# Kernel tuning notes

Hardware: AMD Instinct MI355X
Metric: run time of the kernel (lower is better)

## Reference

```python
import jax, jax.numpy as jnp
import numpy as np

N, D_IN, D_OUT = 8192, 1024, 1024

def setup_inputs() -> dict:
    key = jax.random.key(0)
    k0, k1, k2, k3 = jax.random.split(key, 4)
    scale = 1.0 / np.sqrt(D_IN)
    return {
        "inputs": jax.random.normal(k0, (N, D_IN), dtype=jnp.float32),
        "W_q": jax.random.uniform(k1, (D_IN, D_OUT), jnp.float32, -scale, scale),
        "W_k": jax.random.uniform(k2, (D_IN, D_OUT), jnp.float32, -scale, scale),
        "W_v": jax.random.uniform(k3, (D_IN, D_OUT), jnp.float32, -scale, scale),
    }

def reference(inputs, W_q, W_k, W_v):
    # Linear projections (no bias): [N, d_out]
    q = inputs @ W_q
    k = inputs @ W_k
    v = inputs @ W_v
    d_k = k.shape[-1]
    # Full N x N scores, scaled softmax over last axis
    scores = (q @ k.T) / jnp.sqrt(jnp.asarray(d_k, q.dtype))
    attn = jax.nn.softmax(scores, axis=-1)
    return attn @ v
```

## Files before the change

kernel.cpp:

```cpp
#include <hip/hip_runtime.h>
#include <hip/hip_fp16.h>
#include <stdint.h>


typedef _Float16 half_t;
typedef _Float16 half8 __attribute__((ext_vector_type(8)));
typedef _Float16 half4 __attribute__((ext_vector_type(4)));
typedef float f32x4 __attribute__((ext_vector_type(4)));
typedef int i32x4 __attribute__((ext_vector_type(4)));

#define GLOAD16(gp, lp)                                                        \
  __builtin_amdgcn_global_load_lds(                                            \
      (__attribute__((address_space(1))) void*)(gp),                           \
      (__attribute__((address_space(3))) void*)(lp), 16, 0, 0)

#define BAR() __builtin_amdgcn_s_barrier()
#define VMCNT8() asm volatile("s_waitcnt vmcnt(8)")
#define VMCNT4() asm volatile("s_waitcnt vmcnt(4)")
#define VMCNT0() asm volatile("s_waitcnt vmcnt(0)")

__global__ __launch_bounds__(256) void cast_f32_to_f16(
    const float* __restrict__ in, half_t* __restrict__ out, int n4) {
  int i = blockIdx.x * 256 + threadIdx.x;
  if (i < n4) {
    float4 v = ((const float4*)in)[i];
    half4 o = {(half_t)v.x, (half_t)v.y, (half_t)v.z, (half_t)v.w};
    ((half4*)out)[i] = o;
  }
}

template <typename Tin>
__global__ __launch_bounds__(256) void transpose_cast(
    const Tin* __restrict__ in, int ldin, half_t* __restrict__ out, int ldout,
    int R, int C) {
  __shared__ half_t tile[64][65];
  const int c0 = blockIdx.x * 64, r0 = blockIdx.y * 64;
  const int tx = threadIdx.x & 63, ty = threadIdx.x >> 6;
#pragma unroll
  for (int i = 0; i < 16; i++) {
    int r = ty * 16 + i;
    tile[r][tx] = (half_t)in[(size_t)(r0 + r) * ldin + c0 + tx];
  }
  __syncthreads();
#pragma unroll
  for (int i = 0; i < 16; i++) {
    int c = ty * 16 + i;
    out[(size_t)(c0 + c) * ldout + r0 + tx] = tile[tx][c];
  }
}

__global__ __launch_bounds__(256) void rowsum_recip(
    const float* __restrict__ rowpart, float* __restrict__ rinv, int rows,
    int w4) {
  int r = blockIdx.x * 256 + threadIdx.x;
  if (r < rows) {
    const float4* p = (const float4*)(rowpart + (size_t)r * (w4 * 4));
    float s = 0.f;
    for (int i = 0; i < w4; i++) {
      float4 v = p[i];
      s += v.x + v.y + v.z + v.w;
    }
    rinv[r] = 1.f / s;
  }
}

__global__ __launch_bounds__(256) void reduce_add2h(
    const half8* __restrict__ a, const half8* __restrict__ b,
    float4* __restrict__ o, int n8) {
  int i = blockIdx.x * 256 + threadIdx.x;
  if (i < n8) {
    half8 x = a[i], y = b[i];
    float4 o0, o1;
    o0.x = (float)x[0] + (float)y[0];
    o0.y = (float)x[1] + (float)y[1];
    o0.z = (float)x[2] + (float)y[2];
    o0.w = (float)x[3] + (float)y[3];
    o1.x = (float)x[4] + (float)y[4];
    o1.y = (float)x[5] + (float)y[5];
    o1.z = (float)x[6] + (float)y[6];
    o1.w = (float)x[7] + (float)y[7];
    o[2 * i] = o0;
    o[2 * i + 1] = o1;
  }
}

template <typename To, int MODE>
__global__ __launch_bounds__(512, 2) void gemm256(
    const half_t* __restrict__ A, int lda, const half_t* __restrict__ Bt,
    int ldb, To* __restrict__ C, int ldc, int M, int N, int K, int ychunks,
    int SG, const float* __restrict__ rinv, int8_t* __restrict__ qi8,
    int8_t* __restrict__ ki8) {
  __shared__ __align__(16) char sm[131072];

  const int t = threadIdx.x;
  const int w = t >> 6;
  const int ln = t & 63;

  const int nwg = gridDim.x * gridDim.y;
  const int bid = blockIdx.y * gridDim.x + blockIdx.x;
  const int cpx = nwg >> 3;
  const int q = (bid & 7) * cpx + (bid >> 3);
  const int tiles_y = gridDim.y / ychunks;
  const int per_chunk = gridDim.x * tiles_y;
  const int chunk = q / per_chunk;
  int r_ = q - chunk * per_chunk;
  const int sw = SG * tiles_y;
  const int s_ = r_ / sw;
  r_ -= s_ * sw;
  const int by = r_ / SG;
  const int bx = s_ * SG + (r_ - by * SG);

  A += (size_t)chunk * K;
  Bt += (size_t)chunk * K;
  C += (size_t)chunk * M * ldc;

  const int row0 = by * 256;
  const int col0 = bx * 256;

  const int srow = w * 8 + (ln >> 3);
  const int sslot = (ln & 7) ^ ((ln >> 3) & 7);
  const half_t* Ag = A + (size_t)(row0 + srow) * lda + sslot * 8;
  const half_t* Bg = Bt + (size_t)(col0 + srow) * ldb + sslot * 8;
  const int ldsw = w * 1024;

#define STAGE_AB(kt, bb)                                                       \
  do {                                                                         \
    const half_t* ga_ = Ag + (size_t)(kt) * 64;                                \
    const half_t* gb_ = Bg + (size_t)(kt) * 64;                                \
    GLOAD16(ga_, sm + (bb) + ldsw);                                            \
    GLOAD16(ga_ + 64 * (size_t)lda, sm + (bb) + 8192 + ldsw);                  \
    GLOAD16(ga_ + 128 * (size_t)lda, sm + (bb) + 16384 + ldsw);                \
    GLOAD16(ga_ + 192 * (size_t)lda, sm + (bb) + 24576 + ldsw);                \
    GLOAD16(gb_, sm + (bb) + 32768 + ldsw);                                    \
    GLOAD16(gb_ + 64 * (size_t)ldb, sm + (bb) + 40960 + ldsw);                 \
    GLOAD16(gb_ + 128 * (size_t)ldb, sm + (bb) + 49152 + ldsw);                \
    GLOAD16(gb_ + 192 * (size_t)ldb, sm + (bb) + 57344 + ldsw);                \
  } while (0)

  const int wr = w >> 2;
  const int wc = w & 3;
  const int fr = ln & 15;
  const int kg = ln >> 4;
  const int sx0 = ((kg ^ (fr & 7)) << 4);
  const int sx1 = sx0 ^ 64;
  const int arow = (wr * 128 + fr) * 128;
  const int brow = 32768 + (wc * 64 + fr) * 128;

#define READ_A(MI0, cb)                                                        \
  _Pragma("unroll") for (int mi = 0; mi < 4; mi++) {                           \
    a4[mi][0] = *(const half8*)(sm + (cb) + arow + (MI0 + mi) * 2048 + sx0);   \
    a4[mi][1] = *(const half8*)(sm + (cb) + arow + (MI0 + mi) * 2048 + sx1);   \
  }
#define READ_B(NI, cb)                                                         \
  do {                                                                         \
    b8[NI][0] = *(const half8*)(sm + (cb) + brow + (NI) * 2048 + sx0);         \
    b8[NI][1] = *(const half8*)(sm + (cb) + brow + (NI) * 2048 + sx1);         \
  } while (0)

#define MFMA_Q(MI0, NI0)                                                       \
  __builtin_amdgcn_s_setprio(1);                                               \
  _Pragma("unroll") for (int kk = 0; kk < 2; kk++)                             \
  _Pragma("unroll") for (int mi = 0; mi < 4; mi++)                             \
  _Pragma("unroll") for (int ni = 0; ni < 2; ni++)                             \
      acc[MI0 + mi][NI0 + ni] = __builtin_amdgcn_mfma_f32_16x16x32_f16(        \
          a4[mi][kk], b8[NI0 + ni][kk], acc[MI0 + mi][NI0 + ni], 0, 0, 0);     \
  __builtin_amdgcn_s_setprio(0);

  half8 a4[4][2], b8[4][2];
  f32x4 acc[8][4] = {};

  const int NT = K >> 6;

  STAGE_AB(0, 0);
  STAGE_AB(1, 65536);
  VMCNT8();
  BAR();

#define TILE(tt, cb)                                                           \
  do {                                                                         \
    READ_A(0, cb);                                                             \
    READ_B(0, cb);                                                             \
    READ_B(1, cb);                                                             \
    BAR();                                                                     \
    MFMA_Q(0, 0);                                                              \
    BAR();                                                                     \
    READ_B(2, cb);                                                             \
    READ_B(3, cb);                                                             \
    BAR();                                                                     \
    MFMA_Q(0, 2);                                                              \
    BAR();                                                                     \
    READ_A(4, cb);                                                             \
    BAR();                                                                     \
    MFMA_Q(4, 2);                                                              \
    BAR();                                                                     \
    if ((tt) + 2 < NT) {                                                       \
      STAGE_AB((tt) + 2, cb);                                                  \
      VMCNT8();                                                                \
    } else {                                                                   \
      VMCNT0();                                                                \
    }                                                                          \
    BAR();                                                                     \
    MFMA_Q(4, 0);                                                              \
    BAR();                                                                     \
  } while (0)

  for (int kt = 0; kt < NT; kt += 2) {
    TILE(kt, 0);
    TILE(kt + 1, 65536);
  }

  const int orow = row0 + wr * 128 + (ln >> 4) * 4;
  const int ocol = col0 + wc * 64 + (ln & 15);
  if constexpr (MODE == 2) {
    if (bx < 8) {
      int8_t* qk = bx < 4 ? qi8 : ki8;
      const int cbase = ocol - (bx < 4 ? 0 : 1024);
#pragma unroll
      for (int mi = 0; mi < 8; mi++)
#pragma unroll
        for (int j = 0; j < 4; j++) {
          const size_t r = orow + mi * 16 + j;
#pragma unroll
          for (int ni = 0; ni < 4; ni++) {
            float f = acc[mi][ni][j] * 32.f;
            f = fminf(fmaxf(f, -127.f), 127.f);
            qk[r * 1024 + cbase + ni * 16] = (int8_t)rintf(f);
          }
        }
    } else {
      const int cbase = ocol - 2048;
#pragma unroll
      for (int mi = 0; mi < 8; mi++)
#pragma unroll
        for (int ni = 0; ni < 4; ni++) {
          To* cp = C + (size_t)(orow + mi * 16) * ldc + cbase + ni * 16;
#pragma unroll
          for (int j = 0; j < 4; j++) cp[(size_t)j * ldc] = (To)acc[mi][ni][j];
        }
    }
  } else if constexpr (MODE == 3) {
#pragma unroll
    for (int mi = 0; mi < 8; mi++)
#pragma unroll
      for (int j = 0; j < 4; j++) {
        const size_t r = orow + mi * 16 + j;
        const float s = rinv[r];
#pragma unroll
        for (int ni = 0; ni < 4; ni++)
          C[r * ldc + ocol + ni * 16] = (To)(acc[mi][ni][j] * s);
      }
  } else {
#pragma unroll
    for (int mi = 0; mi < 8; mi++)
#pragma unroll
      for (int ni = 0; ni < 4; ni++) {
        To* cp = C + (size_t)(orow + mi * 16) * ldc + ocol + ni * 16;
#pragma unroll
        for (int j = 0; j < 4; j++) cp[(size_t)j * ldc] = (To)acc[mi][ni][j];
      }
  }
#undef TILE
#undef MFMA_Q
#undef READ_A
#undef READ_B
#undef STAGE_AB
}

__global__ __launch_bounds__(512, 2) void gemm256_i8exp(
    const int8_t* __restrict__ A, int lda, const int8_t* __restrict__ Bt,
    int ldb, half_t* __restrict__ C, int ldc, int K, int SG,
    float* __restrict__ rowpart) {
  __shared__ __align__(16) char sm[65536];

  const int t = threadIdx.x;
  const int w = t >> 6;
  const int ln = t & 63;

  const int nwg = gridDim.x * gridDim.y;
  const int bid = blockIdx.y * gridDim.x + blockIdx.x;
  const int cpx = nwg >> 3;
  const int q = (bid & 7) * cpx + (bid >> 3);
  const int sw = SG * gridDim.y;
  const int s_ = q / sw;
  int r_ = q - s_ * sw;
  const int by = r_ / SG;
  const int bx = s_ * SG + (r_ - by * SG);

  const int row0 = by * 256;
  const int col0 = bx * 256;

  const int rt = w * 16 + (ln >> 2);
  const int sl = (ln & 3) ^ ((rt >> 1) & 3);
  const int8_t* Ag = A + (size_t)(row0 + rt) * lda + sl * 16;
  const int8_t* Bg = Bt + (size_t)(col0 + rt) * ldb + sl * 16;
  const int ldsw = w * 1024;

#define STAGE8(kt, bb)                                                         \
  do {                                                                         \
    const int8_t* ga_ = Ag + (size_t)(kt) * 64;                                \
    const int8_t* gb_ = Bg + (size_t)(kt) * 64;                                \
    GLOAD16(ga_, sm + (bb) + ldsw);                                            \
    GLOAD16(ga_ + 128 * (size_t)lda, sm + (bb) + 8192 + ldsw);                 \
    GLOAD16(gb_, sm + (bb) + 16384 + ldsw);                                    \
    GLOAD16(gb_ + 128 * (size_t)ldb, sm + (bb) + 24576 + ldsw);                \
  } while (0)

  const int wr = w >> 2;
  const int wc = w & 3;
  const int fr = ln & 15;
  const int kg = ln >> 4;
  const int sx = (kg ^ ((fr >> 1) & 3)) << 4;
  const int arow = (wr * 128 + fr) * 64;
  const int brow = 16384 + (wc * 64 + fr) * 64;

#define READ_A8(MI0, cb)                                                       \
  _Pragma("unroll") for (int mi = 0; mi < 4; mi++)                             \
      a8[mi] = *(const i32x4*)(sm + (cb) + arow + (MI0 + mi) * 1024 + sx);
#define READ_B8(NI, cb)                                                        \
  b8v[NI] = *(const i32x4*)(sm + (cb) + brow + (NI) * 1024 + sx);

#define MFMA_Q8(MI0, NI0)                                                      \
  __builtin_amdgcn_s_setprio(1);                                               \
  _Pragma("unroll") for (int mi = 0; mi < 4; mi++)                             \
  _Pragma("unroll") for (int ni = 0; ni < 2; ni++)                             \
      acc[MI0 + mi][NI0 + ni] = __builtin_amdgcn_mfma_i32_16x16x64_i8(         \
          a8[mi], b8v[NI0 + ni], acc[MI0 + mi][NI0 + ni], 0, 0, 0);            \
  __builtin_amdgcn_s_setprio(0);

  i32x4 a8[4], b8v[4];
  i32x4 acc[8][4] = {};

  const int NT = K >> 6;

  STAGE8(0, 0);
  STAGE8(1, 32768);
  VMCNT4();
  BAR();

#define TILE8(tt, cb)                                                          \
  do {                                                                         \
                                                                       \
    READ_A8(0, cb);                                                            \
    READ_B8(0, cb);                                                            \
    READ_B8(1, cb);                                                            \
    READ_B8(2, cb);                                                            \
    READ_B8(3, cb);                                                            \
    MFMA_Q8(0, 0);                                                             \
    MFMA_Q8(0, 2);                                                             \
                                                                       \
    READ_A8(4, cb);                                                            \
    MFMA_Q8(4, 2);                                                             \
    BAR();        \
    if ((tt) + 2 < NT) {                                                       \
      STAGE8((tt) + 2, cb);                                                    \
      MFMA_Q8(4, 0);                                                           \
      VMCNT4();                     \
    } else {                                                                   \
      MFMA_Q8(4, 0);                                                           \
      VMCNT0();                                                                \
    }                                                                          \
    BAR();                             \
  } while (0)

  for (int kt = 0; kt < NT; kt += 2) {
    TILE8(kt, 0);
    TILE8(kt + 1, 32768);
  }

  const int orow = row0 + wr * 128 + (ln >> 4) * 4;
  const int ocol = col0 + wc * 64 + (ln & 15);
  const float sc = 3.0517578125e-5f;
  const int rp_ld = gridDim.x * 4;
#pragma unroll
  for (int mi = 0; mi < 8; mi++) {
#pragma unroll
    for (int j = 0; j < 4; j++) {
      const int r = orow + mi * 16 + j;
      float s = 0.f;
#pragma unroll
      for (int ni = 0; ni < 4; ni++) {
        float e = __expf((float)acc[mi][ni][j] * sc);
        C[(size_t)r * ldc + ocol + ni * 16] = (half_t)e;
        s += e;
      }
      s += __shfl_xor(s, 1);
      s += __shfl_xor(s, 2);
      s += __shfl_xor(s, 4);
      s += __shfl_xor(s, 8);
      if ((ln & 15) == 0) rowpart[(size_t)r * rp_ld + bx * 4 + wc] = s;
    }
  }
#undef TILE8
#undef MFMA_Q8
#undef READ_A8
#undef READ_B8
#undef STAGE8
}

extern "C" void kernel_launch(void* const* d_in, const int* in_sizes, int n_in,
                              void* d_out, int out_size, void* d_ws,
                              size_t ws_size, hipStream_t stream) {
  const float* X = (const float*)d_in[0];
  const float* Wq = (const float*)d_in[1];
  const float* Wk = (const float*)d_in[2];
  const float* Wv = (const float*)d_in[3];
  float* out = (float*)d_out;

  const int N = 8192, D = 1024;

  char* ws = (char*)d_ws;
  half_t* Xh   = (half_t*)(ws);
  half_t* Wth  = (half_t*)(ws + (16ull << 20));
  half_t* Vh   = (half_t*)(ws + (22ull << 20));
  half_t* partH= (half_t*)(ws + (38ull << 20));
  int8_t* Qi8  = (int8_t*)(ws + (70ull << 20));
  int8_t* Ki8  = (int8_t*)(ws + (78ull << 20));
  half_t* Vt   = (half_t*)(ws + (70ull << 20));
  half_t* S    = (half_t*)(ws + (86ull << 20));
  float* rowpart = (float*)ws;
  float* rinv    = (float*)(ws + (4ull << 20));

  cast_f32_to_f16<<<(N * D / 4 + 255) / 256, 256, 0, stream>>>(X, Xh, N * D / 4);

  dim3 tg(D / 64, D / 64);
  transpose_cast<float><<<tg, 256, 0, stream>>>(Wq, D, Wth + 0ull * D * D, D, D, D);
  transpose_cast<float><<<tg, 256, 0, stream>>>(Wk, D, Wth + 1ull * D * D, D, D, D);
  transpose_cast<float><<<tg, 256, 0, stream>>>(Wv, D, Wth + 2ull * D * D, D, D, D);

  gemm256<half_t, 2><<<dim3(3 * D / 256, N / 256), 512, 0, stream>>>(
      Xh, D, Wth, D, Vh, D, N, 3 * D, D, 1, 4, nullptr, Qi8, Ki8);

  gemm256_i8exp<<<dim3(N / 256, N / 256), 512, 0, stream>>>(
      Qi8, D, Ki8, D, S, N, D, 8, rowpart);

  rowsum_recip<<<(N + 255) / 256, 256, 0, stream>>>(rowpart, rinv, N, 32);

  transpose_cast<half_t><<<dim3(D / 64, N / 64), 256, 0, stream>>>(
      Vh, D, Vt, N, N, D);

  gemm256<half_t, 3><<<dim3(D / 256, 2 * N / 256), 512, 0, stream>>>(
      S, N, Vt, N, partH, D, N, D, N / 2, 2, 4, rinv, nullptr, nullptr);

  reduce_add2h<<<(N * D / 8 + 255) / 256, 256, 0, stream>>>(
      (const half8*)partH, (const half8*)(partH + (size_t)N * D), (float4*)out,
      N * D / 8);
}
```

Before: 322.6 us.

## Software-pipeline LDS fragment reads against MFMA in both GEMM mainloops

Restructures the f16 and int8 GEMM inner loops to double-buffer register fragments, so the LDS reads for the next quarter or tile are issued before the current MFMA block runs. It also prefetches the next tile's first A/B fragments right after the staging barrier. Most intra-tile barriers are dropped and replaced with sched_barrier and explicit lgkmcnt waits. This should hide LDS latency behind matrix math and cut barrier stalls, at the cost of more live VGPRs and a risk of lower occupancy or spills.

```diff
diff --git a/kernel.cpp b/kernel.cpp
--- a/kernel.cpp
+++ b/kernel.cpp
@@ -15,6 +15,8 @@
       (__attribute__((address_space(3))) void*)(lp), 16, 0, 0)
 
 #define BAR() __builtin_amdgcn_s_barrier()
+#define SCHED0() __builtin_amdgcn_sched_barrier(0)
+#define LGKM0() asm volatile("s_waitcnt lgkmcnt(0)")
 #define VMCNT8() asm volatile("s_waitcnt vmcnt(8)")
 #define VMCNT4() asm volatile("s_waitcnt vmcnt(4)")
 #define VMCNT0() asm volatile("s_waitcnt vmcnt(0)")
@@ -146,27 +148,22 @@
   const int arow = (wr * 128 + fr) * 128;
   const int brow = 32768 + (wc * 64 + fr) * 128;
 
-#define READ_A(MI0, cb)                                                        \
-  _Pragma("unroll") for (int mi = 0; mi < 4; mi++) {                           \
-    a4[mi][0] = *(const half8*)(sm + (cb) + arow + (MI0 + mi) * 2048 + sx0);   \
-    a4[mi][1] = *(const half8*)(sm + (cb) + arow + (MI0 + mi) * 2048 + sx1);   \
-  }
-#define READ_B(NI, cb)                                                         \
-  do {                                                                         \
-    b8[NI][0] = *(const half8*)(sm + (cb) + brow + (NI) * 2048 + sx0);         \
-    b8[NI][1] = *(const half8*)(sm + (cb) + brow + (NI) * 2048 + sx1);         \
-  } while (0)
-
-#define MFMA_Q(MI0, NI0)                                                       \
+#define RD_A(dst, MI0, cb, SX)                                                 \
+  _Pragma("unroll") for (int mi = 0; mi < 4; mi++) dst[mi] =                   \
+      *(const half8*)(sm + (cb) + arow + ((MI0) + mi) * 2048 + (SX));
+#define RD_B(dst, cb, SX)                                                      \
+  _Pragma("unroll") for (int ni = 0; ni < 4; ni++) dst[ni] =                   \
+      *(const half8*)(sm + (cb) + brow + ni * 2048 + (SX));
+
+#define MM16(MI0, As, Bs)                                                      \
   __builtin_amdgcn_s_setprio(1);                                               \
-  _Pragma("unroll") for (int kk = 0; kk < 2; kk++)                             \
   _Pragma("unroll") for (int mi = 0; mi < 4; mi++)                             \
-  _Pragma("unroll") for (int ni = 0; ni < 2; ni++)                             \
-      acc[MI0 + mi][NI0 + ni] = __builtin_amdgcn_mfma_f32_16x16x32_f16(        \
-          a4[mi][kk], b8[NI0 + ni][kk], acc[MI0 + mi][NI0 + ni], 0, 0, 0);     \
+  _Pragma("unroll") for (int ni = 0; ni < 4; ni++)                             \
+      acc[(MI0) + mi][ni] = __builtin_amdgcn_mfma_f32_16x16x32_f16(            \
+          As[mi], Bs[ni], acc[(MI0) + mi][ni], 0, 0, 0);                       \
   __builtin_amdgcn_s_setprio(0);
 
-  half8 a4[4][2], b8[4][2];
+  half8 Aa[4], Ab[4], Bb0[4], Bb1[4];
   f32x4 acc[8][4] = {};
 
   const int NT = K >> 6;
@@ -175,23 +172,26 @@
   STAGE_AB(1, 65536);
   VMCNT8();
   BAR();
+  RD_A(Aa, 0, 0, sx0);
+  RD_B(Bb0, 0, sx0);
 
 #define TILE(tt, cb)                                                           \
   do {                                                                         \
-    READ_A(0, cb);                                                             \
-    READ_B(0, cb);                                                             \
-    READ_B(1, cb);                                                             \
-    BAR();                                                                     \
-    MFMA_Q(0, 0);                                                              \
-    BAR();                                                                     \
-    READ_B(2, cb);                                                             \
-    READ_B(3, cb);                                                             \
-    BAR();                                                                     \
-    MFMA_Q(0, 2);                                                              \
-    BAR();                                                                     \
-    READ_A(4, cb);                                                             \
-    BAR();                                                                     \
-    MFMA_Q(4, 2);                                                              \
+                                                              \
+    RD_A(Ab, 4, cb, sx0);                                                      \
+    SCHED0();                                                                  \
+    MM16(0, Aa, Bb0);                                                          \
+                                                              \
+    RD_A(Aa, 0, cb, sx1);                                                      \
+    RD_B(Bb1, cb, sx1);                                                        \
+    SCHED0();                                                                  \
+    MM16(4, Ab, Bb0);                                                          \
+                                                              \
+    RD_A(Ab, 4, cb, sx1);                                                      \
+    SCHED0();                                                                  \
+    MM16(0, Aa, Bb1);                                                          \
+                \
+    LGKM0();                                                                   \
     BAR();                                                                     \
     if ((tt) + 2 < NT) {                                                       \
       STAGE_AB((tt) + 2, cb);                                                  \
@@ -200,8 +200,13 @@
       VMCNT0();                                                                \
     }                                                                          \
     BAR();                                                                     \
-    MFMA_Q(4, 0);                                                              \
-    BAR();                                                                     \
+                \
+    if ((tt) + 1 < NT) {                                                       \
+      RD_A(Aa, 0, (cb) ^ 65536, sx0);                                          \
+      RD_B(Bb0, (cb) ^ 65536, sx0);                                            \
+    }                                                                          \
+    SCHED0();                                                                  \
+    MM16(4, Ab, Bb1);                                                          \
   } while (0)
 
   for (int kt = 0; kt < NT; kt += 2) {
@@ -260,9 +265,9 @@
       }
   }
 #undef TILE
-#undef MFMA_Q
-#undef READ_A
-#undef READ_B
+#undef MM16
+#undef RD_A
+#undef RD_B
 #undef STAGE_AB
 }
 
@@ -313,21 +318,22 @@
   const int arow = (wr * 128 + fr) * 64;
   const int brow = 16384 + (wc * 64 + fr) * 64;
 
-#define READ_A8(MI0, cb)                                                       \
-  _Pragma("unroll") for (int mi = 0; mi < 4; mi++)                             \
-      a8[mi] = *(const i32x4*)(sm + (cb) + arow + (MI0 + mi) * 1024 + sx);
-#define READ_B8(NI, cb)                                                        \
-  b8v[NI] = *(const i32x4*)(sm + (cb) + brow + (NI) * 1024 + sx);
-
-#define MFMA_Q8(MI0, NI0)                                                      \
+#define RD_A8(dst, MI0, cb)                                                    \
+  _Pragma("unroll") for (int mi = 0; mi < 4; mi++) dst[mi] =                   \
+      *(const i32x4*)(sm + (cb) + arow + ((MI0) + mi) * 1024 + sx);
+#define RD_B8(dst, cb)                                                         \
+  _Pragma("unroll") for (int ni = 0; ni < 4; ni++) dst[ni] =                   \
+      *(const i32x4*)(sm + (cb) + brow + ni * 1024 + sx);
+
+#define MM16_8(MI0, As, Bs)                                                    \
   __builtin_amdgcn_s_setprio(1);                                               \
   _Pragma("unroll") for (int mi = 0; mi < 4; mi++)                             \
-  _Pragma("unroll") for (int ni = 0; ni < 2; ni++)                             \
-      acc[MI0 + mi][NI0 + ni] = __builtin_amdgcn_mfma_i32_16x16x64_i8(         \
-          a8[mi], b8v[NI0 + ni], acc[MI0 + mi][NI0 + ni], 0, 0, 0);            \
+  _Pragma("unroll") for (int ni = 0; ni < 4; ni++)                             \
+      acc[(MI0) + mi][ni] = __builtin_amdgcn_mfma_i32_16x16x64_i8(             \
+          As[mi], Bs[ni], acc[(MI0) + mi][ni], 0, 0, 0);                       \
   __builtin_amdgcn_s_setprio(0);
 
-  i32x4 a8[4], b8v[4];
+  i32x4 Aa8[4], Ab8[4], B0s[4], B1s[4];
   i32x4 acc[8][4] = {};
 
   const int NT = K >> 6;
@@ -336,35 +342,37 @@
   STAGE8(1, 32768);
   VMCNT4();
   BAR();
-
-#define TILE8(tt, cb)                                                          \
+  RD_A8(Aa8, 0, 0);
+  RD_B8(B0s, 0);
+
+#define TILE8(tt, cb, Bc, Bn)                                                  \
   do {                                                                         \
-                                                                       \
-    READ_A8(0, cb);                                                            \
-    READ_B8(0, cb);                                                            \
-    READ_B8(1, cb);                                                            \
-    READ_B8(2, cb);                                                            \
-    READ_B8(3, cb);                                                            \
-    MFMA_Q8(0, 0);                                                             \
-    MFMA_Q8(0, 2);                                                             \
-                                                                       \
-    READ_A8(4, cb);                                                            \
-    MFMA_Q8(4, 2);                                                             \
-    BAR();        \
+                                                                 \
+    RD_A8(Ab8, 4, cb);                                                         \
+    SCHED0();                                                                  \
+    MM16_8(0, Aa8, Bc);                                                        \
+                                                                 \
+    LGKM0();                                                                   \
+    BAR();                                                                     \
     if ((tt) + 2 < NT) {                                                       \
       STAGE8((tt) + 2, cb);                                                    \
-      MFMA_Q8(4, 0);                                                           \
-      VMCNT4();                     \
+      VMCNT4();                                                                \
     } else {                                                                   \
-      MFMA_Q8(4, 0);                                                           \
       VMCNT0();                                                                \
     }                                                                          \
-    BAR();                             \
+    BAR();                                                                     \
+                       \
+    if ((tt) + 1 < NT) {                                                       \
+      RD_A8(Aa8, 0, (cb) ^ 32768);                                             \
+      RD_B8(Bn, (cb) ^ 32768);                                                 \
+    }                                                                          \
+    SCHED0();                                                                  \
+    MM16_8(4, Ab8, Bc);                                                        \
   } while (0)
 
   for (int kt = 0; kt < NT; kt += 2) {
-    TILE8(kt, 0);
-    TILE8(kt + 1, 32768);
+    TILE8(kt, 0, B0s, B1s);
+    TILE8(kt + 1, 32768, B1s, B0s);
   }
 
   const int orow = row0 + wr * 128 + (ln >> 4) * 4;
@@ -391,9 +399,9 @@
     }
   }
 #undef TILE8
-#undef MFMA_Q8
-#undef READ_A8
-#undef READ_B8
+#undef MM16_8
+#undef RD_A8
+#undef RD_B8
 #undef STAGE8
 }
 
```

After: 573.5 us. 77.8% more time.

## Write V transposed from projection epilogue and use dedicated K=32 f16 PV GEMM

Applied to the files above, without the earlier changes.

The projection GEMM epilogue now writes V directly in transposed layout as 4-element half vectors, which removes the separate V transpose kernel and its extra pass over memory. The P·V product moves to a new gemm256_h32 kernel that uses the 16x16x32 f16 MFMA with a double-buffered 32-wide K tile and applies the row reciprocal in the epilogue. The transposed V stores are strided by N, so they may coalesce poorly. The new kernel's pipelining also differs from the generic gemm256 path.

```diff
diff --git a/kernel.cpp b/kernel.cpp
--- a/kernel.cpp
+++ b/kernel.cpp
@@ -228,27 +228,16 @@
           }
         }
     } else {
-      const int cbase = ocol - 2048;
 #pragma unroll
       for (int mi = 0; mi < 8; mi++)
 #pragma unroll
         for (int ni = 0; ni < 4; ni++) {
-          To* cp = C + (size_t)(orow + mi * 16) * ldc + cbase + ni * 16;
-#pragma unroll
-          for (int j = 0; j < 4; j++) cp[(size_t)j * ldc] = (To)acc[mi][ni][j];
+          const int c = ocol - 2048 + ni * 16;
+          half4 v = {(half_t)acc[mi][ni][0], (half_t)acc[mi][ni][1],
+                     (half_t)acc[mi][ni][2], (half_t)acc[mi][ni][3]};
+          *(half4*)(C + (size_t)c * ldc + orow + mi * 16) = v;
         }
     }
-  } else if constexpr (MODE == 3) {
-#pragma unroll
-    for (int mi = 0; mi < 8; mi++)
-#pragma unroll
-      for (int j = 0; j < 4; j++) {
-        const size_t r = orow + mi * 16 + j;
-        const float s = rinv[r];
-#pragma unroll
-        for (int ni = 0; ni < 4; ni++)
-          C[r * ldc + ocol + ni * 16] = (To)(acc[mi][ni][j] * s);
-      }
   } else {
 #pragma unroll
     for (int mi = 0; mi < 8; mi++)
@@ -264,6 +253,134 @@
 #undef READ_A
 #undef READ_B
 #undef STAGE_AB
+}
+
+__global__ __launch_bounds__(512, 2) void gemm256_h32(
+    const half_t* __restrict__ A, int lda, const half_t* __restrict__ Bt,
+    int ldb, half_t* __restrict__ C, int ldc, int M, int K, int ychunks,
+    int SG, const float* __restrict__ rinv) {
+  __shared__ __align__(16) char sm[65536];
+
+  const int t = threadIdx.x;
+  const int w = t >> 6;
+  const int ln = t & 63;
+
+  const int nwg = gridDim.x * gridDim.y;
+  const int bid = blockIdx.y * gridDim.x + blockIdx.x;
+  const int cpx = nwg >> 3;
+  const int q = (bid & 7) * cpx + (bid >> 3);
+  const int tiles_y = gridDim.y / ychunks;
+  const int per_chunk = gridDim.x * tiles_y;
+  const int chunk = q / per_chunk;
+  int r_ = q - chunk * per_chunk;
+  const int sw = SG * tiles_y;
+  const int s_ = r_ / sw;
+  r_ -= s_ * sw;
+  const int by = r_ / SG;
+  const int bx = s_ * SG + (r_ - by * SG);
+
+  A += (size_t)chunk * K;
+  Bt += (size_t)chunk * K;
+  C += (size_t)chunk * M * ldc;
+
+  const int row0 = by * 256;
+  const int col0 = bx * 256;
+
+  const int rt = w * 16 + (ln >> 2);
+  const int sl = (ln & 3) ^ ((rt >> 1) & 3);
+  const half_t* Ag = A + (size_t)(row0 + rt) * lda + sl * 8;
+  const half_t* Bg = Bt + (size_t)(col0 + rt) * ldb + sl * 8;
+  const int ldsw = w * 1024;
+
+#define STAGEH(kt, bb)                                                         \
+  do {                                                                         \
+    const half_t* ga_ = Ag + (size_t)(kt) * 32;                                \
+    const half_t* gb_ = Bg + (size_t)(kt) * 32;                                \
+    GLOAD16(ga_, sm + (bb) + ldsw);                                            \
+    GLOAD16(ga_ + 128 * (size_t)lda, sm + (bb) + 8192 + ldsw);                 \
+    GLOAD16(gb_, sm + (bb) + 16384 + ldsw);                                    \
+    GLOAD16(gb_ + 128 * (size_t)ldb, sm + (bb) + 24576 + ldsw);                \
+  } while (0)
+
+  const int wr = w >> 2;
+  const int wc = w & 3;
+  const int fr = ln & 15;
+  const int kg = ln >> 4;
+  const int sx = (kg ^ ((fr >> 1) & 3)) << 4;
+  const int arow = (wr * 128 + fr) * 64;
+  const int brow = 16384 + (wc * 64 + fr) * 64;
+
+#define RDH_A(MI0, cb)                                                         \
+  _Pragma("unroll") for (int mi = 0; mi < 4; mi++)                             \
+      ah[mi] = *(const half8*)(sm + (cb) + arow + ((MI0) + mi) * 1024 + sx);
+#define RDH_B(NI, cb)                                                          \
+  bh[NI] = *(const half8*)(sm + (cb) + brow + (NI) * 1024 + sx);
+
+#define MMH_Q(MI0, NI0)                                                        \
+  __builtin_amdgcn_s_setprio(1);                                               \
+  _Pragma("unroll") for (int mi = 0; mi < 4; mi++)                             \
+  _Pragma("unroll") for (int ni = 0; ni < 2; ni++)                             \
+      acc[(MI0) + mi][(NI0) + ni] = __builtin_amdgcn_mfma_f32_16x16x32_f16(    \
+          ah[mi], bh[(NI0) + ni], acc[(MI0) + mi][(NI0) + ni], 0, 0, 0);       \
+  __builtin_amdgcn_s_setprio(0);
+
+  half8 ah[4], bh[4];
+  f32x4 acc[8][4] = {};
+
+  const int NT = K >> 5;
+
+  STAGEH(0, 0);
+  STAGEH(1, 32768);
+  VMCNT4();
+  BAR();
+
+#define TILEH(tt, cb)                                                          \
+  do {                                                                         \
+                                                                       \
+    RDH_A(0, cb);                                                              \
+    RDH_B(0, cb);                                                              \
+    RDH_B(1, cb);                                                              \
+    RDH_B(2, cb);                                                              \
+    RDH_B(3, cb);                                                              \
+    MMH_Q(0, 0);                                                               \
+    MMH_Q(0, 2);                                                               \
+                                                                       \
+    RDH_A(4, cb);                                                              \
+    MMH_Q(4, 2);                                                               \
+    BAR();                    \
+    if ((tt) + 2 < NT) {                                                       \
+      STAGEH((tt) + 2, cb);                                                    \
+      MMH_Q(4, 0);                                                             \
+      VMCNT4();                     \
+    } else {                                                                   \
+      MMH_Q(4, 0);                                                             \
+      VMCNT0();                                                                \
+    }                                                                          \
+    BAR();                                          \
+  } while (0)
+
+  for (int kt = 0; kt < NT; kt += 2) {
+    TILEH(kt, 0);
+    TILEH(kt + 1, 32768);
+  }
+
+  const int orow = row0 + wr * 128 + (ln >> 4) * 4;
+  const int ocol = col0 + wc * 64 + (ln & 15);
+#pragma unroll
+  for (int mi = 0; mi < 8; mi++)
+#pragma unroll
+    for (int j = 0; j < 4; j++) {
+      const size_t r = orow + mi * 16 + j;
+      const float s = rinv[r];
+#pragma unroll
+      for (int ni = 0; ni < 4; ni++)
+        C[r * ldc + ocol + ni * 16] = (half_t)(acc[mi][ni][j] * s);
+    }
+#undef TILEH
+#undef MMH_Q
+#undef RDH_A
+#undef RDH_B
+#undef STAGEH
 }
 
 __global__ __launch_bounds__(512, 2) void gemm256_i8exp(
@@ -411,11 +528,10 @@
   char* ws = (char*)d_ws;
   half_t* Xh   = (half_t*)(ws);
   half_t* Wth  = (half_t*)(ws + (16ull << 20));
-  half_t* Vh   = (half_t*)(ws + (22ull << 20));
+  half_t* Vt   = (half_t*)(ws + (22ull << 20));
   half_t* partH= (half_t*)(ws + (38ull << 20));
   int8_t* Qi8  = (int8_t*)(ws + (70ull << 20));
   int8_t* Ki8  = (int8_t*)(ws + (78ull << 20));
-  half_t* Vt   = (half_t*)(ws + (70ull << 20));
   half_t* S    = (half_t*)(ws + (86ull << 20));
   float* rowpart = (float*)ws;
   float* rinv    = (float*)(ws + (4ull << 20));
@@ -428,18 +544,15 @@
   transpose_cast<float><<<tg, 256, 0, stream>>>(Wv, D, Wth + 2ull * D * D, D, D, D);
 
   gemm256<half_t, 2><<<dim3(3 * D / 256, N / 256), 512, 0, stream>>>(
-      Xh, D, Wth, D, Vh, D, N, 3 * D, D, 1, 4, nullptr, Qi8, Ki8);
+      Xh, D, Wth, D, Vt, N, N, 3 * D, D, 1, 4, nullptr, Qi8, Ki8);
 
   gemm256_i8exp<<<dim3(N / 256, N / 256), 512, 0, stream>>>(
       Qi8, D, Ki8, D, S, N, D, 8, rowpart);
 
   rowsum_recip<<<(N + 255) / 256, 256, 0, stream>>>(rowpart, rinv, N, 32);
 
-  transpose_cast<half_t><<<dim3(D / 64, N / 64), 256, 0, stream>>>(
-      Vh, D, Vt, N, N, D);
-
-  gemm256<half_t, 3><<<dim3(D / 256, 2 * N / 256), 512, 0, stream>>>(
-      S, N, Vt, N, partH, D, N, D, N / 2, 2, 4, rinv, nullptr, nullptr);
+  gemm256_h32<<<dim3(D / 256, 2 * N / 256), 512, 0, stream>>>(
+      S, N, Vt, N, partH, D, N, N / 2, 2, 4, rinv);
 
   reduce_add2h<<<(N * D / 8 + 255) / 256, 256, 0, stream>>>(
       (const half8*)partH, (const half8*)(partH + (size_t)N * D), (float4*)out,
```

After: 320.1 us. About the same (-0.8%).
